# Performance work log

Hardware: AMD Instinct MI355X
Metric: run time of the kernel (lower is better)

Reference implementation:

```python
import jax, jax.numpy as jnp
import numpy as np

K = 20
BN_EPS = 1e-5
NEG_SLOPE = 0.2


def knn_idx(x, k):
    # x: [B, C, N]; returns indices of k nearest neighbors per point: [B, N, k]
    sq = jnp.sum(x * x, axis=1)                      # [B, N]
    inner = jnp.einsum('bcn,bcm->bnm', x, x)         # [B, N, N]
    dist = sq[:, :, None] + sq[:, None, :] - 2.0 * inner  # squared distances
    _, idx = jax.lax.top_k(-dist, k)                 # smallest distances
    return idx


def get_graph_feature(x, k):
    # x: [B, C, N] -> [B, 2C, N, k]
    idx = knn_idx(x, k)                               # [B, N, k]
    gather = lambda xb, ib: xb[:, ib]                 # [C,N] x [N,k] -> [C,N,k]
    feature = jax.vmap(gather)(x, idx)                # [B, C, N, k]
    xk = jnp.broadcast_to(x[:, :, :, None], feature.shape)
    return jnp.concatenate([feature - xk, xk], axis=1)  # [B, 2C, N, k]


def setup_inputs() -> dict:
    key = jax.random.key(0)
    k1, k2 = jax.random.split(key)
    B, C, N = 8, 64, 4096
    x = jax.random.normal(k1, (B, C, N), dtype=jnp.float32)
    W = jax.random.normal(k2, (64, 2 * C), dtype=jnp.float32) * (1.0 / np.sqrt(2 * C))
    gamma = jnp.ones((64,), dtype=jnp.float32)
    beta = jnp.zeros((64,), dtype=jnp.float32)
    return {"x": x, "W": W, "gamma": gamma, "beta": beta}


def reference(x, W, gamma, beta):
    g = get_graph_feature(x, K)                       # [B, 2C, N, k]
    y = jnp.einsum('oc,bcnk->bonk', W, g)             # 1x1 conv, no bias
    # BatchNorm2d (training-mode batch statistics) over (B, N, k) per channel
    mean = jnp.mean(y, axis=(0, 2, 3), keepdims=True)
    var = jnp.var(y, axis=(0, 2, 3), keepdims=True)
    y = (y - mean) * jax.lax.rsqrt(var + BN_EPS)
    y = y * gamma[None, :, None, None] + beta[None, :, None, None]
    # LeakyReLU(0.2)
    y = jnp.where(y >= 0, y, NEG_SLOPE * y)
    # max over neighbors
    return jnp.max(y, axis=-1)                        # [B, out, N]
```

## Files before the change

kernel.cpp:

```cpp
#include <hip/hip_runtime.h>
#include <hip/hip_bf16.h>
#include <float.h>

#define BATCH 8
#define CDIM 64
#define NPTS 4096
#define KNN 20
#define KSEL 32
#define BUFCAP 128
#define BN_EPS 1e-5f
#define NEG_SLOPE 0.2f

typedef __attribute__((ext_vector_type(8))) short short8;
typedef __attribute__((ext_vector_type(4))) float float4v;
typedef unsigned short ushort;
typedef unsigned int uint;
typedef unsigned long long ull;

__device__ __forceinline__ ushort f2bf(float f) {
    uint u = __float_as_uint(f);
    u += 0x7FFF + ((u >> 16) & 1);
    return (ushort)(u >> 16);
}
__device__ __forceinline__ int mbcnt64(ull m) {
    int c = __builtin_amdgcn_mbcnt_lo((uint)m, 0);
    return __builtin_amdgcn_mbcnt_hi((uint)(m >> 32), c);
}

__device__ __forceinline__ uint select33_truncate(uint* __restrict__ buf,
                                                  int& cnt, int lane) {
    uint e0 = 0xFFFFFFFFu, e1 = 0xFFFFFFFFu;
    if (lane < cnt) e0 = buf[lane];
    if (64 + lane < cnt) e1 = buf[64 + lane];
    uint p = 0;
    for (int bit = 31; bit >= 0; --bit) {
        uint t = p | (1u << bit);
        ull mA = __ballot(e0 < t);
        ull mB = __ballot(e1 < t);
        if (__popcll(mA) + __popcll(mB) < 33) p = t;
    }
    ull mA = __ballot(e0 < p);
    ull mB = __ballot(e1 < p);
    int pA = __popcll(mA);
    int r0 = mbcnt64(mA);
    int r1 = pA + mbcnt64(mB);
    if (e0 < p) buf[r0] = e0;
    if (e1 < p) buf[r1] = e1;
    cnt = pA + __popcll(mB);
    return p;
}

__device__ __forceinline__ void scan_append(float dwv, float base, int idx,
                                            uint& tau, int& cnt,
                                            uint* __restrict__ buf, int lane) {
    float dval = fmaxf(fmaf(-2.f, dwv, base), 0.f);
    uint key = (__float_as_uint(dval) & 0xFFFFF000u) | (uint)idx;
    ull mask = __ballot(key < tau);
    if (mask) {
        int c = __popcll(mask);
        if (cnt + c > BUFCAP) {
            tau = select33_truncate(buf, cnt, lane);
            mask = __ballot(key < tau);
            c = __popcll(mask);
        }
        if (c) {
            int rank = mbcnt64(mask);
            if (key < tau) buf[cnt + rank] = key;
            cnt += c;
        }
    }
}

__global__ void k_prep(const float* __restrict__ x,
                       float* __restrict__ xt,
                       ushort* __restrict__ xh,
                       float* __restrict__ sq) {
    int gid = blockIdx.x * 256 + threadIdx.x;
    int b = gid >> 12;
    int n = gid & (NPTS - 1);
    const float* xb = x + (size_t)b * CDIM * NPTS + n;
    float acc = 0.f;
    float4* xtv = (float4*)(xt + ((size_t)gid << 6));
    uint2* xhp = (uint2*)(xh + ((size_t)gid << 6));
    #pragma unroll
    for (int q = 0; q < 16; ++q) {
        float v[4]; ushort h[4];
        #pragma unroll
        for (int j = 0; j < 4; ++j) {
            float tv = xb[(q * 4 + j) * NPTS];
            v[j] = tv;
            acc = fmaf(tv, tv, acc);
            h[j] = f2bf(tv);
        }
        xtv[q] = make_float4(v[0], v[1], v[2], v[3]);
        uint2 ph;
        ph.x = (uint)h[0] | ((uint)h[1] << 16);
        ph.y = (uint)h[2] | ((uint)h[3] << 16);
        xhp[q] = ph;
    }
    sq[gid] = acc;
}

__global__ void k_pz(const float* __restrict__ xt, const float* __restrict__ W,
                     float* __restrict__ pt, float* __restrict__ zt) {
    int b  = blockIdx.x >> 6;
    int n0 = (blockIdx.x & 63) << 6;
    int lane = threadIdx.x & 63;
    int w = threadIdx.x >> 6;
    int n = n0 + lane;
    size_t rowoff = ((size_t)(b * NPTS + n)) << 6;
    const float4* xrow = (const float4*)(xt + rowoff);
    float acc1[16], acc2[16];
    #pragma unroll
    for (int i = 0; i < 16; ++i) { acc1[i] = 0.f; acc2[i] = 0.f; }
    #pragma unroll
    for (int cg = 0; cg < 4; ++cg) {
        float xv[16];
        #pragma unroll
        for (int q = 0; q < 4; ++q) {
            float4 t = xrow[cg * 4 + q];
            xv[q*4] = t.x; xv[q*4+1] = t.y; xv[q*4+2] = t.z; xv[q*4+3] = t.w;
        }
        #pragma unroll
        for (int oi = 0; oi < 16; ++oi) {
            int o = (w << 4) + oi;
            const float* wr = W + o * 128 + cg * 16;
            float a1 = acc1[oi], a2 = acc2[oi];
            #pragma unroll
            for (int j = 0; j < 16; ++j) {
                a1 = fmaf(wr[j],      xv[j], a1);
                a2 = fmaf(wr[64 + j], xv[j], a2);
            }
            acc1[oi] = a1; acc2[oi] = a2;
        }
    }
    float4* pv = (float4*)(pt + rowoff + (w << 4));
    float4* zv = (float4*)(zt + rowoff + (w << 4));
    #pragma unroll
    for (int q = 0; q < 4; ++q) {
        pv[q] = make_float4(acc1[q*4], acc1[q*4+1], acc1[q*4+2], acc1[q*4+3]);
        zv[q] = make_float4(acc2[q*4]   - acc1[q*4],
                            acc2[q*4+1] - acc1[q*4+1],
                            acc2[q*4+2] - acc1[q*4+2],
                            acc2[q*4+3] - acc1[q*4+3]);
    }
}

__global__ void __launch_bounds__(512, 8) k_knn(
        const ushort* __restrict__ xh,
        const float* __restrict__ sq, ushort* __restrict__ knn32) {
    __shared__ float dw[2][2][16][68];
    __shared__ uint rowbuf[32 * BUFCAP];

    int tid  = threadIdx.x;
    int wv   = tid >> 6;
    int lane = tid & 63;
    int g    = wv >> 2;
    int t    = wv & 3;
    int b    = blockIdx.x >> 7;
    int r0   = ((blockIdx.x & 127) << 5) + (g << 4);
    int col  = lane & 15;
    int quad = lane >> 4;

    size_t arow = ((size_t)(b * NPTS + r0 + col)) << 6;
    short8 ah0 = *(const short8*)(xh + arow + quad * 8);
    short8 ah1 = *(const short8*)(xh + arow + 32 + quad * 8);

    const ushort* xhb = xh + (((size_t)b * NPTS) << 6);
    const float* sqb = sq + b * NPTS;
    const ushort* fbase = xhb + (((size_t)((t << 4) + col)) << 6) + (quad << 3);

    uint tau[4];
    int cnt[4];
    float sqr[4];
    uint* wbuf = rowbuf + ((wv << 2) * BUFCAP);
    #pragma unroll
    for (int r = 0; r < 4; ++r) {
        tau[r] = 0xFFFFFFFFu; cnt[r] = 0;
        sqr[r] = sqb[r0 + (t << 2) + r];
    }

    short8 fA0 = *(const short8*)fbase;
    short8 fA1 = *(const short8*)(fbase + 32);
    short8 fB0, fB1;
    float sv_cur = 0.f;
    float sv_nxt = sqb[lane];

    auto step = [&](int c, int q, short8& f0, short8& f1,
                    short8& nf0, short8& nf1) {
        if (c + 1 < 64) {
            const ushort* p = fbase + (((size_t)(c + 1)) << 12);
            nf0 = *(const short8*)p;
            nf1 = *(const short8*)(p + 32);
        }
        float sv_tmp = (c + 1 < 64) ? sqb[((c + 1) << 6) + lane] : 0.f;

        float4v acc = {0.f, 0.f, 0.f, 0.f};
        acc = __builtin_amdgcn_mfma_f32_16x16x32_bf16(ah0, f0, acc, 0, 0, 0);
        acc = __builtin_amdgcn_mfma_f32_16x16x32_bf16(ah1, f1, acc, 0, 0, 0);
        #pragma unroll
        for (int r = 0; r < 4; ++r)
            dw[q][g][(quad << 2) + r][(t << 4) + col] = acc[r];

        if (c > 0) {
            int m0 = (c - 1) << 6;
            #pragma unroll
            for (int r = 0; r < 4; ++r) {
                float dv = dw[q ^ 1][g][(t << 2) + r][lane];
                scan_append(dv, sv_cur + sqr[r], m0 + lane, tau[r], cnt[r],
                            wbuf + r * BUFCAP, lane);
            }
        }
        sv_cur = sv_nxt;
        sv_nxt = sv_tmp;

        __builtin_amdgcn_sched_barrier(0);
        asm volatile("s_waitcnt lgkmcnt(0)" ::: "memory");
        __builtin_amdgcn_s_barrier();
        __builtin_amdgcn_sched_barrier(0);
    };

    for (int c = 0; c < 64; c += 2) {
        step(c,     0, fA0, fA1, fB0, fB1);
        step(c + 1, 1, fB0, fB1, fA0, fA1);
    }

    {
        int m0 = 63 << 6;
        #pragma unroll
        for (int r = 0; r < 4; ++r) {
            float dv = dw[1][g][(t << 2) + r][lane];
            scan_append(dv, sv_cur + sqr[r], m0 + lane, tau[r], cnt[r],
                        wbuf + r * BUFCAP, lane);
        }
    }

    #pragma unroll
    for (int r = 0; r < 4; ++r) {
        select33_truncate(wbuf + r * BUFCAP, cnt[r], lane);
        if (lane < KSEL) {
            uint e = wbuf[r * BUFCAP + lane];
            knn32[(size_t)(b * NPTS + r0 + (t << 2) + r) * KSEL + lane] =
                (ushort)(e & 0xFFFu);
        }
    }
}

__global__ void __launch_bounds__(256) k_refine(
        const float* __restrict__ xt, const float* __restrict__ sq,
        const ushort* __restrict__ knn32, int* __restrict__ idx20) {
    int wvid = (blockIdx.x << 2) + (threadIdx.x >> 6);
    int lane = threadIdx.x & 63;
    int half = lane >> 5;
    int sl   = lane & 31;
    int row  = (wvid << 1) + half;
    int b = row >> 12;
    int cand = knn32[(size_t)row * KSEL + sl];
    const float4* xc = (const float4*)(xt + ((size_t)(b * NPTS + cand) << 6));
    const float4* xr = (const float4*)(xt + ((size_t)row << 6));
    float acc = 0.f;
    #pragma unroll
    for (int q = 0; q < 16; ++q) {
        float4 a = xr[q], c = xc[q];
        acc = fmaf(a.x, c.x, acc); acc = fmaf(a.y, c.y, acc);
        acc = fmaf(a.z, c.z, acc); acc = fmaf(a.w, c.w, acc);
    }
    float d = fmaf(-2.f, acc, sq[b * NPTS + cand]);
    int rank = 0;
    int base = half << 5;
    #pragma unroll
    for (int j = 0; j < KSEL; ++j) {
        float dj = __shfl(d, base + j);
        int   cj = __shfl(cand, base + j);
        rank += ((dj < d) || (dj == d && cj < cand)) ? 1 : 0;
    }
    if (rank < KNN)
        idx20[(size_t)row * KNN + rank] = cand;
}

__global__ void k_gather(const float* __restrict__ pt, const float* __restrict__ zt,
                         const int* __restrict__ idxin,
                         float* __restrict__ tmax, float* __restrict__ tmin,
                         float* __restrict__ S1, float* __restrict__ S2) {
    __shared__ float red1[4][64];
    __shared__ float red2[4][64];
    int b  = blockIdx.x >> 6;
    int n0 = (blockIdx.x & 63) << 6;
    int lane = threadIdx.x & 63;
    int w = threadIdx.x >> 6;
    float cs1 = 0.f, cs2 = 0.f;
    for (int i = 0; i < 16; ++i) {
        int n = n0 + (w << 4) + i;
        int base = b * NPTS + n;
        int ibase = __builtin_amdgcn_readfirstlane(base * KNN);
        const int* ip = idxin + ibase;
        float mx = -FLT_MAX, mn = FLT_MAX, s1 = 0.f, s2 = 0.f;
        #pragma unroll
        for (int k = 0; k < KNN; ++k) {
            int colp = ip[k];
            float v = pt[(((size_t)(b * NPTS + colp)) << 6) + lane];
            mx = fmaxf(mx, v); mn = fminf(mn, v);
            s1 += v; s2 = fmaf(v, v, s2);
        }
        float z = zt[(((size_t)base) << 6) + lane];
        tmax[(((size_t)base) << 6) + lane] = mx + z;
        tmin[(((size_t)base) << 6) + lane] = mn + z;
        cs1 += s1 + (float)KNN * z;
        cs2 += s2 + 2.f * z * s1 + (float)KNN * z * z;
    }
    red1[w][lane] = cs1;
    red2[w][lane] = cs2;
    __syncthreads();
    if (threadIdx.x < 64) {
        float t1 = red1[0][lane] + red1[1][lane] + red1[2][lane] + red1[3][lane];
        float t2 = red2[0][lane] + red2[1][lane] + red2[2][lane] + red2[3][lane];
        atomicAdd(&S1[lane], t1);
        atomicAdd(&S2[lane], t2);
    }
}

__global__ void k_final(const float* __restrict__ tmax, const float* __restrict__ tmin,
                        const float* __restrict__ S1, const float* __restrict__ S2,
                        const float* __restrict__ gamma, const float* __restrict__ beta,
                        float* __restrict__ out) {
    __shared__ float smx[64][65];
    __shared__ float smn[64][65];
    int b  = blockIdx.x >> 6;
    int n0 = (blockIdx.x & 63) << 6;
    int lane = threadIdx.x & 63;
    int w = threadIdx.x >> 6;
    #pragma unroll
    for (int i = 0; i < 16; ++i) {
        int nl = (i << 2) + w;
        size_t off = (((size_t)(b * NPTS + n0 + nl)) << 6) + lane;
        smx[nl][lane] = tmax[off];
        smn[nl][lane] = tmin[off];
    }
    __syncthreads();
    const float inv_cnt = 1.0f / ((float)BATCH * NPTS * KNN);
    #pragma unroll
    for (int i = 0; i < 16; ++i) {
        int o = (i << 2) + w;
        float s1 = S1[o], s2 = S2[o];
        float mean = s1 * inv_cnt;
        float var = fmaf(-mean, mean, s2 * inv_cnt);
        float rs = rsqrtf(var + BN_EPS);
        float sc = gamma[o] * rs;
        float sh = beta[o] - mean * sc;
        float tv = (sc >= 0.f) ? smx[lane][o] : smn[lane][o];
        float y = fmaf(tv, sc, sh);
        y = (y >= 0.f) ? y : NEG_SLOPE * y;
        out[((size_t)(b * 64 + o)) * NPTS + n0 + lane] = y;
    }
}

extern "C" void kernel_launch(void* const* d_in, const int* in_sizes, int n_in,
                              void* d_out, int out_size, void* d_ws, size_t ws_size,
                              hipStream_t stream) {
    const float* x     = (const float*)d_in[0];
    const float* W     = (const float*)d_in[1];
    const float* gamma = (const float*)d_in[2];
    const float* beta  = (const float*)d_in[3];
    float* out = (float*)d_out;

    float* ws = (float*)d_ws;
    const size_t SECT = (size_t)BATCH * NPTS * 64;
    float*  xt    = ws;
    float*  pt    = ws + SECT;
    float*  zt    = ws + 2 * SECT;
    float*  sq    = ws + 3 * SECT;
    float*  S1    = ws + 3 * SECT + 32768;
    float*  S2    = S1 + 64;
    int*    idx20 = (int*)(ws + 3 * SECT + 32768 + 128);
    float*  uA    = ws + 3 * SECT + 32768 + 128 + 655360;
    ushort* xh    = (ushort*)uA;
    ushort* knn32 = (ushort*)(uA + SECT / 2);
    float*  tmx   = uA;
    float*  tmn   = uA + SECT;

    hipMemsetAsync(S1, 0, 2 * 64 * sizeof(float), stream);
    k_prep  <<<dim3((BATCH * NPTS) / 256), dim3(256), 0, stream>>>(x, xt, xh, sq);
    k_pz    <<<dim3(BATCH * (NPTS / 64)), dim3(256), 0, stream>>>(xt, W, pt, zt);
    k_knn   <<<dim3(1024), dim3(512), 0, stream>>>(xh, sq, knn32);
    k_refine<<<dim3((BATCH * NPTS) / 8), dim3(256), 0, stream>>>(xt, sq, knn32, idx20);
    k_gather<<<dim3(BATCH * (NPTS / 64)), dim3(256), 0, stream>>>(pt, zt, idx20, tmx, tmn, S1, S2);
    k_final <<<dim3(BATCH * (NPTS / 64)), dim3(256), 0, stream>>>(tmx, tmn, S1, S2, gamma, beta, out);
}
```

Before: 362.5 us.

## Make kNN distance tiles wave-private to drop block barriers

The kNN kernel now has each wave own 16 query rows and compute the full 16x64 distance tile for each chunk itself with four MFMA pairs. The result is staged in wave-private LDS, which removes the per-step block-wide s_barrier and the cross-wave double buffer. The block shrinks to 256 threads with 512 blocks, and the candidate buffer capacity drops from 128 to 96. The cost is more registers (16 thresholds and counters plus 16 prefetched fragments), possible loss of occupancy, and less room in the candidate buffer before truncation.

```diff
diff --git a/kernel.cpp b/kernel.cpp
--- a/kernel.cpp
+++ b/kernel.cpp
@@ -7,7 +7,7 @@
 #define NPTS 4096
 #define KNN 20
 #define KSEL 32
-#define BUFCAP 128
+#define BUFCAP 96
 #define BN_EPS 1e-5f
 #define NEG_SLOPE 0.2f
 
@@ -146,21 +146,22 @@
     }
 }
 
-__global__ void __launch_bounds__(512, 8) k_knn(
+__global__ void __launch_bounds__(256) k_knn(
         const ushort* __restrict__ xh,
         const float* __restrict__ sq, ushort* __restrict__ knn32) {
-    __shared__ float dw[2][2][16][68];
-    __shared__ uint rowbuf[32 * BUFCAP];
+    __shared__ float dwW[4][16][68];
+    __shared__ uint rowbufW[4][16 * BUFCAP];
 
     int tid  = threadIdx.x;
     int wv   = tid >> 6;
     int lane = tid & 63;
-    int g    = wv >> 2;
-    int t    = wv & 3;
-    int b    = blockIdx.x >> 7;
-    int r0   = ((blockIdx.x & 127) << 5) + (g << 4);
+    int b    = blockIdx.x >> 6;
+    int r0   = ((blockIdx.x & 63) << 6) + (wv << 4);
     int col  = lane & 15;
     int quad = lane >> 4;
+
+    float (* __restrict__ dw)[68] = dwW[wv];
+    uint* __restrict__ wbuf = rowbufW[wv];
 
     size_t arow = ((size_t)(b * NPTS + r0 + col)) << 6;
     short8 ah0 = *(const short8*)(xh + arow + quad * 8);
@@ -168,79 +169,69 @@
 
     const ushort* xhb = xh + (((size_t)b * NPTS) << 6);
     const float* sqb = sq + b * NPTS;
-    const ushort* fbase = xhb + (((size_t)((t << 4) + col)) << 6) + (quad << 3);
-
-    uint tau[4];
-    int cnt[4];
-    float sqr[4];
-    uint* wbuf = rowbuf + ((wv << 2) * BUFCAP);
-    #pragma unroll
-    for (int r = 0; r < 4; ++r) {
+
+    uint tau[16];
+    int cnt[16];
+    float sqr[16];
+    #pragma unroll
+    for (int r = 0; r < 16; ++r) {
         tau[r] = 0xFFFFFFFFu; cnt[r] = 0;
-        sqr[r] = sqb[r0 + (t << 2) + r];
-    }
-
-    short8 fA0 = *(const short8*)fbase;
-    short8 fA1 = *(const short8*)(fbase + 32);
-    short8 fB0, fB1;
-    float sv_cur = 0.f;
-    float sv_nxt = sqb[lane];
-
-    auto step = [&](int c, int q, short8& f0, short8& f1,
-                    short8& nf0, short8& nf1) {
+        sqr[r] = sqb[r0 + r];
+    }
+
+    short8 fE[8], fO[8];
+    #pragma unroll
+    for (int j = 0; j < 4; ++j) {
+        const ushort* p = xhb + (((size_t)(16 * j + col)) << 6) + (quad << 3);
+        fE[2*j]   = *(const short8*)p;
+        fE[2*j+1] = *(const short8*)(p + 32);
+    }
+    float sv_cur = sqb[lane];
+
+    auto step = [&](int c, short8 (&f)[8], short8 (&nf)[8]) {
         if (c + 1 < 64) {
-            const ushort* p = fbase + (((size_t)(c + 1)) << 12);
-            nf0 = *(const short8*)p;
-            nf1 = *(const short8*)(p + 32);
-        }
-        float sv_tmp = (c + 1 < 64) ? sqb[((c + 1) << 6) + lane] : 0.f;
-
-        float4v acc = {0.f, 0.f, 0.f, 0.f};
-        acc = __builtin_amdgcn_mfma_f32_16x16x32_bf16(ah0, f0, acc, 0, 0, 0);
-        acc = __builtin_amdgcn_mfma_f32_16x16x32_bf16(ah1, f1, acc, 0, 0, 0);
-        #pragma unroll
-        for (int r = 0; r < 4; ++r)
-            dw[q][g][(quad << 2) + r][(t << 4) + col] = acc[r];
-
-        if (c > 0) {
-            int m0 = (c - 1) << 6;
+            int m1 = (c + 1) << 6;
             #pragma unroll
-            for (int r = 0; r < 4; ++r) {
-                float dv = dw[q ^ 1][g][(t << 2) + r][lane];
-                scan_append(dv, sv_cur + sqr[r], m0 + lane, tau[r], cnt[r],
-                            wbuf + r * BUFCAP, lane);
+            for (int j = 0; j < 4; ++j) {
+                const ushort* p =
+                    xhb + (((size_t)(m1 + 16 * j + col)) << 6) + (quad << 3);
+                nf[2*j]   = *(const short8*)p;
+                nf[2*j+1] = *(const short8*)(p + 32);
             }
         }
-        sv_cur = sv_nxt;
-        sv_nxt = sv_tmp;
-
-        __builtin_amdgcn_sched_barrier(0);
-        asm volatile("s_waitcnt lgkmcnt(0)" ::: "memory");
-        __builtin_amdgcn_s_barrier();
-        __builtin_amdgcn_sched_barrier(0);
-    };
-
-    for (int c = 0; c < 64; c += 2) {
-        step(c,     0, fA0, fA1, fB0, fB1);
-        step(c + 1, 1, fB0, fB1, fA0, fA1);
-    }
-
-    {
-        int m0 = 63 << 6;
-        #pragma unroll
-        for (int r = 0; r < 4; ++r) {
-            float dv = dw[1][g][(t << 2) + r][lane];
+        float sv_nxt = (c + 1 < 64) ? sqb[((c + 1) << 6) + lane] : 0.f;
+
+        #pragma unroll
+        for (int j = 0; j < 4; ++j) {
+            float4v acc = {0.f, 0.f, 0.f, 0.f};
+            acc = __builtin_amdgcn_mfma_f32_16x16x32_bf16(ah0, f[2*j],   acc, 0, 0, 0);
+            acc = __builtin_amdgcn_mfma_f32_16x16x32_bf16(ah1, f[2*j+1], acc, 0, 0, 0);
+            #pragma unroll
+            for (int r = 0; r < 4; ++r)
+                dw[(quad << 2) + r][16 * j + col] = acc[r];
+        }
+
+        int m0 = c << 6;
+        #pragma unroll
+        for (int r = 0; r < 16; ++r) {
+            float dv = dw[r][lane];
             scan_append(dv, sv_cur + sqr[r], m0 + lane, tau[r], cnt[r],
                         wbuf + r * BUFCAP, lane);
         }
-    }
-
-    #pragma unroll
-    for (int r = 0; r < 4; ++r) {
+        sv_cur = sv_nxt;
+    };
+
+    for (int c = 0; c < 64; c += 2) {
+        step(c,     fE, fO);
+        step(c + 1, fO, fE);
+    }
+
+    #pragma unroll
+    for (int r = 0; r < 16; ++r) {
         select33_truncate(wbuf + r * BUFCAP, cnt[r], lane);
         if (lane < KSEL) {
             uint e = wbuf[r * BUFCAP + lane];
-            knn32[(size_t)(b * NPTS + r0 + (t << 2) + r) * KSEL + lane] =
+            knn32[(size_t)(b * NPTS + r0 + r) * KSEL + lane] =
                 (ushort)(e & 0xFFFu);
         }
     }
@@ -381,7 +372,7 @@
     hipMemsetAsync(S1, 0, 2 * 64 * sizeof(float), stream);
     k_prep  <<<dim3((BATCH * NPTS) / 256), dim3(256), 0, stream>>>(x, xt, xh, sq);
     k_pz    <<<dim3(BATCH * (NPTS / 64)), dim3(256), 0, stream>>>(xt, W, pt, zt);
-    k_knn   <<<dim3(1024), dim3(512), 0, stream>>>(xh, sq, knn32);
+    k_knn   <<<dim3(BATCH * (NPTS / 64)), dim3(256), 0, stream>>>(xh, sq, knn32);
     k_refine<<<dim3((BATCH * NPTS) / 8), dim3(256), 0, stream>>>(xt, sq, knn32, idx20);
     k_gather<<<dim3(BATCH * (NPTS / 64)), dim3(256), 0, stream>>>(pt, zt, idx20, tmx, tmn, S1, S2);
     k_final <<<dim3(BATCH * (NPTS / 64)), dim3(256), 0, stream>>>(tmx, tmn, S1, S2, gamma, beta, out);
```

Result: slower. 433.0 us (+19.4%).
